# Kernel optimization log

Measured on AMD Instinct MI355X. Metric: run time of the kernel, lower is better.

Reference implementation:

```python
import jax, jax.numpy as jnp
import numpy as np

RES = 28      # input feature-map resolution
RES2 = 14     # ceil(RES/2) after downsample
NH = 8        # num_heads
KD = 16       # key_dim
D = 64        # attn_ratio * key_dim (per-head value dim)
DH = 512      # D * NH
N = RES * RES
N2 = RES2 * RES2


def _rel_idx():
    # Matches tf.meshgrid default 'xy' indexing in set_attention_bias_idxs.
    r = RES
    kp = np.stack(np.meshgrid(np.arange(r), np.arange(r), indexing='xy')).reshape(2, -1)
    qp = np.stack(np.meshgrid(np.arange(0, r, 2), np.arange(0, r, 2), indexing='xy')).reshape(2, -1)
    rel = np.abs(qp[:, :, None] - kp[:, None, :])
    return jnp.asarray(rel[0] * r + rel[1], dtype=jnp.int32)  # [N2, N]

REL_IDX = _rel_idx()


def _dw_stride2(x, w, b):
    # Depthwise 3x3 conv, stride 2, TF 'SAME' padding. w: [3,3,1,C]
    c = x.shape[-1]
    y = jax.lax.conv_general_dilated(
        x, w, window_strides=(2, 2), padding='SAME',
        dimension_numbers=('NHWC', 'HWIO', 'NHWC'), feature_group_count=c)
    return y + b


def setup_inputs() -> dict:
    key = jax.random.key(0)
    ks = jax.random.split(key, 10)
    f = jnp.float32
    C, OUT = 384, 768
    return {
        'x': jax.random.normal(ks[0], (64, RES, RES, C), f),
        'q_local_w': jax.random.normal(ks[1], (3, 3, 1, C), f) * 0.1,
        'q_local_b': jnp.zeros((C,), f),
        'q_proj_w': jax.random.normal(ks[2], (C, NH * KD), f) * 0.05,
        'q_proj_b': jnp.zeros((NH * KD,), f),
        'q_bn_s': jnp.ones((NH * KD,), f),
        'q_bn_b': jnp.zeros((NH * KD,), f),
        'k_w': jax.random.normal(ks[3], (C, NH * KD), f) * 0.05,
        'k_b': jnp.zeros((NH * KD,), f),
        'k_bn_s': jnp.ones((NH * KD,), f),
        'k_bn_b': jnp.zeros((NH * KD,), f),
        'v_w': jax.random.normal(ks[4], (C, DH), f) * 0.05,
        'v_b': jnp.zeros((DH,), f),
        'v_bn_s': jnp.ones((DH,), f),
        'v_bn_b': jnp.zeros((DH,), f),
        'vloc_w': jax.random.normal(ks[5], (3, 3, 1, DH), f) * 0.1,
        'vloc_b': jnp.zeros((DH,), f),
        'vloc_bn_s': jnp.ones((DH,), f),
        'vloc_bn_b': jnp.zeros((DH,), f),
        'proj_w': jax.random.normal(ks[6], (DH, OUT), f) * 0.05,
        'proj_b': jnp.zeros((OUT,), f),
        'proj_bn_s': jnp.ones((OUT,), f),
        'proj_bn_b': jnp.zeros((OUT,), f),
        'attn_bias': jax.random.normal(ks[7], (NH, N), f) * 0.1,
    }


def reference(x, q_local_w, q_local_b, q_proj_w, q_proj_b, q_bn_s, q_bn_b,
              k_w, k_b, k_bn_s, k_bn_b, v_w, v_b, v_bn_s, v_bn_b,
              vloc_w, vloc_b, vloc_bn_s, vloc_bn_b,
              proj_w, proj_b, proj_bn_s, proj_bn_b, attn_bias):
    B = x.shape[0]
    scale = KD ** -0.5
    # LGQuery: depthwise-conv local branch + 1x1 avg-pool (stride-2 subsample)
    q = _dw_stride2(x, q_local_w, q_local_b) + x[:, ::2, ::2, :]
    q = (q @ q_proj_w + q_proj_b) * q_bn_s + q_bn_b          # [B,14,14,128]
    k = (x @ k_w + k_b) * k_bn_s + k_bn_b                    # [B,28,28,128]
    v = (x @ v_w + v_b) * v_bn_s + v_bn_b                    # [B,28,28,512]
    v_local = _dw_stride2(v, vloc_w, vloc_b) * vloc_bn_s + vloc_bn_b  # [B,14,14,512]
    qh = q.reshape(B, N2, NH, KD).transpose(0, 2, 1, 3)      # [B,H,N2,KD]
    kh = k.reshape(B, N, NH, KD).transpose(0, 2, 3, 1)       # [B,H,KD,N]
    vh = v.reshape(B, N, NH, D).transpose(0, 2, 1, 3)        # [B,H,N,D]
    attn = (qh @ kh) * scale + attn_bias[:, REL_IDX]         # [B,H,N2,N]
    attn = jax.nn.softmax(attn, axis=-1)
    out = (attn @ vh).transpose(0, 2, 1, 3).reshape(B, RES2, RES2, DH)
    out = out + v_local
    # proj: Activation(None) is identity -> 1x1 conv + BN(inference)
    return (out @ proj_w + proj_b) * proj_bn_s + proj_bn_b   # [B,14,14,768]
```

## Files before the change

### kernel.cpp

```cpp
#include <hip/hip_runtime.h>
#include <cstdint>

#define RES    28
#define RES2   14
#define NHEAD  8
#define KDIM   16
#define DV     64
#define DHID   512
#define NSEQ   784
#define N2SEQ  196
#define BATCH  64
#define CIN    384

typedef unsigned short u16;
typedef short  short8_t __attribute__((ext_vector_type(8)));
typedef float  f32x4  __attribute__((ext_vector_type(4)));
typedef u16    us4    __attribute__((ext_vector_type(4)));
typedef u16    us8    __attribute__((ext_vector_type(8)));

__device__ __forceinline__ u16 f2bf(float f) {
    uint32_t u = __float_as_uint(f);
    return (u16)((u + 0x7fffu + ((u >> 16) & 1u)) >> 16);
}
__device__ __forceinline__ float bf2f(u16 h) {
    return __uint_as_float(((uint32_t)h) << 16);
}

#define PREP_N (49152 + 196608 + 49152 + 393216 + 1920 + 256)
__global__ __launch_bounds__(256)
void prep_kernel(const float* __restrict__ k_w, const float* __restrict__ v_w,
                 const float* __restrict__ q_proj_w, const float* __restrict__ proj_w,
                 const float* __restrict__ k_b, const float* __restrict__ v_b,
                 const float* __restrict__ k_bn_s, const float* __restrict__ v_bn_s,
                 const float* __restrict__ k_bn_b, const float* __restrict__ v_bn_b,
                 const float* __restrict__ q_bn_s, const float* __restrict__ q_bn_b,
                 u16* __restrict__ kvwt, u16* __restrict__ qwt, u16* __restrict__ pwt,
                 float* __restrict__ kv_eps, float* __restrict__ qsb)
{
    int i = blockIdx.x * 256 + threadIdx.x;
    if (i >= PREP_N) return;
    if (i < 49152) {
        int n = i / 384, k = i % 384;
        kvwt[i] = f2bf(k_w[(size_t)k * 128 + n]);
        return;
    }
    i -= 49152;
    if (i < 196608) {
        int n = i / 384, k = i % 384;
        kvwt[49152 + i] = f2bf(v_w[(size_t)k * 512 + n]);
        return;
    }
    i -= 196608;
    if (i < 49152) {
        int n = i / 384, k = i % 384;
        qwt[i] = f2bf(q_proj_w[(size_t)k * 128 + n]);
        return;
    }
    i -= 49152;
    if (i < 393216) {
        int n = i / 512, k = i % 512;
        pwt[i] = f2bf(proj_w[(size_t)k * 768 + n]);
        return;
    }
    i -= 393216;
    if (i < 1920) {
        int which = i / 640, j = i % 640;
        const float* a = which == 0 ? (j < 128 ? k_b : v_b)
                       : which == 1 ? (j < 128 ? k_bn_s : v_bn_s)
                                    : (j < 128 ? k_bn_b : v_bn_b);
        kv_eps[i] = a[j < 128 ? j : j - 128];
        return;
    }
    i -= 1920;
    qsb[i] = 0.25f * (i < 128 ? q_bn_s[i] : q_bn_b[i - 128]);
}

__global__ __launch_bounds__(256)
void biasC_kernel(const float* __restrict__ bias, float* __restrict__ biasC)
{
    int tid = blockIdx.x * 256 + threadIdx.x;
    if (tid >= NHEAD * 13 * 4 * 13 * 64) return;
    int lane = tid & 63;
    int rem  = tid >> 6;
    int qt = rem % 13; rem /= 13;
    int ks = rem % 4;  rem /= 4;
    int ti = rem % 13;
    int h  = rem / 13;
    int col = lane & 15, quad = lane >> 4;
    int q = qt * 16 + col;
    float4 out;
    float* po = &out.x;
    #pragma unroll
    for (int r = 0; r < 4; ++r) {
        int key = ti * 64 + ks * 16 + quad * 4 + r;
        float v;
        if (key >= NSEQ || q >= N2SEQ) {
            v = -1e30f;
        } else {
            int pi = q / 14, pj = q % 14;
            int ku = key / 28, kw = key % 28;
            int d0 = 2 * pj - kw; if (d0 < 0) d0 = -d0;
            int d1 = 2 * pi - ku; if (d1 < 0) d1 = -d1;
            v = bias[h * NSEQ + d0 * 28 + d1];
        }
        po[r] = v;
    }
    ((float4*)biasC)[tid] = out;
}

#define TM 128
#define TN 128
#define TK 32

template<int OUT_MODE, int A_FP32>
__global__ __launch_bounds__(256)
void gemm_mfma_kernel(const void* __restrict__ Av, const u16* __restrict__ Bt,
                      const float* __restrict__ bias, const float* __restrict__ scale,
                      const float* __restrict__ shift, void* __restrict__ outp,
                      u16* __restrict__ out2, int M, int N, int K, int rpb)
{
    __shared__ u16 As[TM * TK];
    __shared__ u16 Bs[TN * TK];

    const int t  = threadIdx.x;
    const int w  = t >> 6;
    const int li = t & 63;
    const int wm = w >> 1, wn = w & 1;
    const int bm = blockIdx.x * TM;
    const int bn = blockIdx.y * TN;
    const int m16 = li & 15;
    const int kg  = li >> 4;

    f32x4 acc[4][4];
    #pragma unroll
    for (int i = 0; i < 4; ++i)
        #pragma unroll
        for (int j = 0; j < 4; ++j) acc[i][j] = (f32x4)0.0f;

    for (int k0 = 0; k0 < K; k0 += TK) {
        #pragma unroll
        for (int i = 0; i < 2; ++i) {
            int c   = (w * 2 + i) * 64 + li;
            int row = c >> 2, kc = c & 3;
            if (A_FP32) {
                const float* ag = (const float*)Av + (size_t)(bm + row) * K + k0 + kc * 8;
                float4 a0 = *(const float4*)ag;
                float4 a1 = *(const float4*)(ag + 4);
                us8 vv;
                vv[0] = f2bf(a0.x); vv[1] = f2bf(a0.y); vv[2] = f2bf(a0.z); vv[3] = f2bf(a0.w);
                vv[4] = f2bf(a1.x); vv[5] = f2bf(a1.y); vv[6] = f2bf(a1.z); vv[7] = f2bf(a1.w);
                *(us8*)&As[(size_t)row * TK + kc * 8] = vv;
            } else {
                const u16* ag = (const u16*)Av + (size_t)(bm + row) * K + k0 + kc * 8;
                char* la = (char*)As + (size_t)(w * 2 + i) * 64 * 16;
                __builtin_amdgcn_global_load_lds(
                    (const __attribute__((address_space(1))) void*)ag,
                    (__attribute__((address_space(3))) void*)la, 16, 0, 0);
            }
            const u16* bg = Bt + (size_t)(bn + row) * K + k0 + kc * 8;
            char* lb = (char*)Bs + (size_t)(w * 2 + i) * 64 * 16;
            __builtin_amdgcn_global_load_lds(
                (const __attribute__((address_space(1))) void*)bg,
                (__attribute__((address_space(3))) void*)lb, 16, 0, 0);
        }
        __syncthreads();

        short8_t af[4], bf[4];
        #pragma unroll
        for (int mi = 0; mi < 4; ++mi)
            af[mi] = *(const short8_t*)&As[(wm * 64 + mi * 16 + m16) * TK + kg * 8];
        #pragma unroll
        for (int ni = 0; ni < 4; ++ni)
            bf[ni] = *(const short8_t*)&Bs[(wn * 64 + ni * 16 + m16) * TK + kg * 8];

        #pragma unroll
        for (int mi = 0; mi < 4; ++mi)
            #pragma unroll
            for (int ni = 0; ni < 4; ++ni)
                acc[mi][ni] = __builtin_amdgcn_mfma_f32_16x16x32_bf16(
                    af[mi], bf[ni], acc[mi][ni], 0, 0, 0);
        __syncthreads();
    }

    #pragma unroll
    for (int ni = 0; ni < 4; ++ni) {
        const int col = bn + wn * 64 + ni * 16 + m16;
        const float bi = bias[col], sc = scale[col], sh = shift[col];
        #pragma unroll
        for (int mi = 0; mi < 4; ++mi) {
            const int rbase = bm + wm * 64 + mi * 16 + kg * 4;
            #pragma unroll
            for (int r = 0; r < 4; ++r) {
                float val = (acc[mi][ni][r] + bi) * sc + sh;
                const int row = rbase + r;
                if (OUT_MODE == 0) {
                    ((float*)outp)[(size_t)row * N + col] = val;
                } else if (OUT_MODE == 1) {
                    ((u16*)outp)[(size_t)row * N + col] = f2bf(val);
                } else if (OUT_MODE == 2) {
                    int bb = row / rpb, tok = row % rpb;
                    int hh = col >> 4;
                    ((u16*)outp)[((size_t)(bb * NHEAD + hh) * rpb + tok) * 16 + (col & 15)] = f2bf(val);
                } else {
                    if (bn < 128) {
                        int bb = row / NSEQ, tok = row % NSEQ;
                        int hh = col >> 4;
                        ((u16*)outp)[((size_t)(bb * NHEAD + hh) * NSEQ + tok) * 16 + (col & 15)] = f2bf(val);
                    } else {
                        out2[(size_t)row * DHID + (col - 128)] = f2bf(val);
                    }
                }
            }
        }
    }
}

__global__ __launch_bounds__(256)
void qin_kernel(const float* __restrict__ x, const float* __restrict__ w,
                const float* __restrict__ b, u16* __restrict__ qin)
{
    const int C4 = CIN / 4;
    int idx = blockIdx.x * 256 + threadIdx.x;
    if (idx >= BATCH * RES2 * RES2 * C4) return;
    int c4 = idx % C4;
    int r  = idx / C4;
    int j  = r % RES2; r /= RES2;
    int i  = r % RES2;
    int bb = r / RES2;

    const float4* x4 = (const float4*)x;
    const float4* w4 = (const float4*)w;
    float4 acc = make_float4(0.f, 0.f, 0.f, 0.f);
    #pragma unroll
    for (int dy = 0; dy < 3; ++dy) {
        int iy = 2 * i + dy;
        if (iy >= RES) continue;
        #pragma unroll
        for (int dx = 0; dx < 3; ++dx) {
            int ix = 2 * j + dx;
            if (ix >= RES) continue;
            float4 xv = x4[((size_t)(bb * RES + iy) * RES + ix) * C4 + c4];
            float4 wv = w4[(dy * 3 + dx) * C4 + c4];
            acc.x += xv.x * wv.x; acc.y += xv.y * wv.y;
            acc.z += xv.z * wv.z; acc.w += xv.w * wv.w;
        }
    }
    float4 bv = ((const float4*)b)[c4];
    float4 xs = x4[((size_t)(bb * RES + 2 * i) * RES + 2 * j) * C4 + c4];
    us4 o;
    o.x = f2bf(acc.x + bv.x + xs.x);
    o.y = f2bf(acc.y + bv.y + xs.y);
    o.z = f2bf(acc.z + bv.z + xs.z);
    o.w = f2bf(acc.w + bv.w + xs.w);
    ((us4*)qin)[idx] = o;
}

__global__ __launch_bounds__(256)
void vloc_kernel(const u16* __restrict__ v, const float* __restrict__ w,
                 const float* __restrict__ b, const float* __restrict__ s,
                 const float* __restrict__ sh, u16* __restrict__ out)
{
    const int C4 = DHID / 4;
    int idx = blockIdx.x * 256 + threadIdx.x;
    if (idx >= BATCH * RES2 * RES2 * C4) return;
    int c4 = idx % C4;
    int r  = idx / C4;
    int j  = r % RES2; r /= RES2;
    int i  = r % RES2;
    int bb = r / RES2;

    const us4* v4 = (const us4*)v;
    const float4* w4 = (const float4*)w;
    float4 acc = make_float4(0.f, 0.f, 0.f, 0.f);
    #pragma unroll
    for (int dy = 0; dy < 3; ++dy) {
        int iy = 2 * i + dy;
        if (iy >= RES) continue;
        #pragma unroll
        for (int dx = 0; dx < 3; ++dx) {
            int ix = 2 * j + dx;
            if (ix >= RES) continue;
            us4 xu = v4[((size_t)(bb * RES + iy) * RES + ix) * C4 + c4];
            float4 wv = w4[(dy * 3 + dx) * C4 + c4];
            acc.x += bf2f(xu.x) * wv.x; acc.y += bf2f(xu.y) * wv.y;
            acc.z += bf2f(xu.z) * wv.z; acc.w += bf2f(xu.w) * wv.w;
        }
    }
    float4 bv = ((const float4*)b)[c4];
    float4 sv = ((const float4*)s)[c4];
    float4 hv = ((const float4*)sh)[c4];
    us4 o;
    o.x = f2bf((acc.x + bv.x) * sv.x + hv.x);
    o.y = f2bf((acc.y + bv.y) * sv.y + hv.y);
    o.z = f2bf((acc.z + bv.z) * sv.z + hv.z);
    o.w = f2bf((acc.w + bv.w) * sv.w + hv.w);
    ((us4*)out)[idx] = o;
}

__global__ __launch_bounds__(256)
void vt_transpose_kernel(const u16* __restrict__ vbuf, u16* __restrict__ vt)
{
    __shared__ u16 tile[64][66];
    const int t  = threadIdx.x;
    const int b  = blockIdx.x;
    const int k0 = blockIdx.y * 64;
    const int h  = blockIdx.z;

    {
        int kr = t >> 2, cc = (t & 3) * 16;
        int key = k0 + kr;
        if (key < NSEQ) {
            const u16* src = vbuf + ((size_t)b * NSEQ + key) * DHID + h * 64 + cc;
            us8 v0 = *(const us8*)src;
            us8 v1 = *(const us8*)(src + 8);
            #pragma unroll
            for (int i = 0; i < 8; ++i) { tile[kr][cc + i] = v0[i]; tile[kr][cc + 8 + i] = v1[i]; }
        }
    }
    __syncthreads();
    {
        int cr = t >> 2, kc = (t & 3) * 16;
        if (k0 + kc < NSEQ) {
            us8 o0, o1;
            #pragma unroll
            for (int i = 0; i < 8; ++i) { o0[i] = tile[kc + i][cr]; o1[i] = tile[kc + 8 + i][cr]; }
            u16* dst = vt + (((size_t)b * NHEAD + h) * 64 + cr) * NSEQ + k0 + kc;
            *(us8*)dst = o0;
            *(us8*)(dst + 8) = o1;
        }
    }
}

__global__ __launch_bounds__(256, 2)
void attn_mfma_kernel(const u16* __restrict__ q, const u16* __restrict__ k,
                      const u16* __restrict__ vt, const float* __restrict__ biasC,
                      u16* __restrict__ io)
{
    __shared__ u16 Ks[64 * 16];
    __shared__ u16 Vs[64 * 68];

    const int t    = threadIdx.x;
    const int w    = t >> 6;
    const int lane = t & 63;
    const int col  = lane & 15;
    const int quad = lane >> 4;
    const int par = blockIdx.x & 1;
    const int bhx = blockIdx.x >> 1;
    const int h  = bhx >> 6;
    const int b  = bhx & 63;
    const int bh = b * NHEAD + h;

    short8_t qf[2];
    #pragma unroll
    for (int i = 0; i < 2; ++i) {
        int qt = w + 4 * (par * 2 + i);
        qf[i] = (short8_t)0;
        if (qt < 13 && quad < 2) {
            int qq = qt * 16 + col; if (qq > 195) qq = 195;
            qf[i] = *(const short8_t*)(q + ((size_t)bh * N2SEQ + qq) * 16 + quad * 8);
        }
    }

    f32x4 O[2][4];
    float m[2], l[2];
    #pragma unroll
    for (int i = 0; i < 2; ++i) {
        m[i] = -3e38f; l[i] = 0.f;
        #pragma unroll
        for (int ns = 0; ns < 4; ++ns) O[i][ns] = (f32x4)0.0f;
    }

    const u16* vtb = vt + (size_t)bh * 64 * NSEQ;
    const u16* kb  = k + (size_t)bh * NSEQ * 16;

    for (int ti = 0; ti < 13; ++ti) {
        const int t0 = ti * 64;
        if (w < 2) {
            int c = w * 64 + lane;
            int tok = t0 + (c >> 1); if (tok > 783) tok = 783;
            const u16* src = kb + (size_t)tok * 16 + (c & 1) * 8;
            char* dst = (char*)Ks + w * 1024;
            __builtin_amdgcn_global_load_lds(
                (const __attribute__((address_space(1))) void*)src,
                (__attribute__((address_space(3))) void*)dst, 16, 0, 0);
        }
        {
            int d = t >> 2, part = t & 3;
            const u16* src = vtb + (size_t)d * NSEQ;
            u16* dst = Vs + d * 68 + part * 16;
            int kk = t0 + part * 16;
            int k0a = kk     > 776 ? 776 : kk;
            int k1a = kk + 8 > 776 ? 776 : kk + 8;
            us8 v0 = *(const us8*)(src + k0a);
            us8 v1 = *(const us8*)(src + k1a);
            us4 a, bb2, c2, d2;
            a.x = v0[0]; a.y = v0[1]; a.z = v0[2]; a.w = v0[3];
            bb2.x = v0[4]; bb2.y = v0[5]; bb2.z = v0[6]; bb2.w = v0[7];
            c2.x = v1[0]; c2.y = v1[1]; c2.z = v1[2]; c2.w = v1[3];
            d2.x = v1[4]; d2.y = v1[5]; d2.z = v1[6]; d2.w = v1[7];
            *(us4*)(dst)      = a;
            *(us4*)(dst + 4)  = bb2;
            *(us4*)(dst + 8)  = c2;
            *(us4*)(dst + 12) = d2;
        }
        __syncthreads();

        short8_t kf[4];
        #pragma unroll
        for (int ks = 0; ks < 4; ++ks) {
            kf[ks] = (short8_t)0;
            if (quad < 2)
                kf[ks] = *(const short8_t*)&Ks[(ks * 16 + col) * 16 + quad * 8];
        }
        short8_t vf[4][2];
        #pragma unroll
        for (int ns = 0; ns < 4; ++ns)
            #pragma unroll
            for (int pr = 0; pr < 2; ++pr) {
                const u16* vrow = &Vs[(ns * 16 + col) * 68 + pr * 32 + quad * 4];
                us4 v0 = *(const us4*)vrow;
                us4 v1 = *(const us4*)(vrow + 16);
                short8_t vv;
                vv[0] = (short)v0.x; vv[1] = (short)v0.y; vv[2] = (short)v0.z; vv[3] = (short)v0.w;
                vv[4] = (short)v1.x; vv[5] = (short)v1.y; vv[6] = (short)v1.z; vv[7] = (short)v1.w;
                vf[ns][pr] = vv;
            }

        #pragma unroll
        for (int i = 0; i < 2; ++i) {
            int qt = w + 4 * (par * 2 + i);
            if (qt < 13) {
                f32x4 S[4];
                #pragma unroll
                for (int ks = 0; ks < 4; ++ks) {
                    f32x4 c = *(const f32x4*)(biasC +
                        ((((size_t)h * 13 + ti) * 4 + ks) * 13 + qt) * 256 + lane * 4);
                    S[ks] = __builtin_amdgcn_mfma_f32_16x16x32_bf16(kf[ks], qf[i], c, 0, 0, 0);
                }
                float p[16];
                float mt = -3e38f;
                #pragma unroll
                for (int ks = 0; ks < 4; ++ks)
                    #pragma unroll
                    for (int r = 0; r < 4; ++r) {
                        float lg = S[ks][r];
                        p[ks * 4 + r] = lg;
                        mt = fmaxf(mt, lg);
                    }
                mt = fmaxf(mt, __shfl_xor(mt, 16));
                mt = fmaxf(mt, __shfl_xor(mt, 32));
                float mnew = fmaxf(m[i], mt);
                float alpha = __expf(m[i] - mnew);
                m[i] = mnew;
                float s = 0.f;
                #pragma unroll
                for (int j = 0; j < 16; ++j) { p[j] = __expf(p[j] - mnew); s += p[j]; }
                s += __shfl_xor(s, 16);
                s += __shfl_xor(s, 32);
                l[i] = l[i] * alpha + s;

                float ar[4];
                #pragma unroll
                for (int r = 0; r < 4; ++r) ar[r] = __shfl(alpha, quad * 4 + r);
                #pragma unroll
                for (int ns = 0; ns < 4; ++ns)
                    #pragma unroll
                    for (int r = 0; r < 4; ++r) O[i][ns][r] *= ar[r];

                short8_t pf[2];
                #pragma unroll
                for (int pr = 0; pr < 2; ++pr)
                    #pragma unroll
                    for (int j = 0; j < 8; ++j)
                        pf[pr][j] = (short)f2bf(p[(2 * pr + (j >> 2)) * 4 + (j & 3)]);

                #pragma unroll
                for (int ns = 0; ns < 4; ++ns)
                    #pragma unroll
                    for (int pr = 0; pr < 2; ++pr)
                        O[i][ns] = __builtin_amdgcn_mfma_f32_16x16x32_bf16(
                            pf[pr], vf[ns][pr], O[i][ns], 0, 0, 0);
            }
        }
        __syncthreads();
    }

    #pragma unroll
    for (int i = 0; i < 2; ++i) {
        int qt = w + 4 * (par * 2 + i);
        if (qt < 13) {
            float linv = 1.0f / l[i];
            float lr[4];
            #pragma unroll
            for (int r = 0; r < 4; ++r) lr[r] = __shfl(linv, quad * 4 + r);
            #pragma unroll
            for (int ns = 0; ns < 4; ++ns)
                #pragma unroll
                for (int r = 0; r < 4; ++r) {
                    int q2 = qt * 16 + quad * 4 + r;
                    if (q2 < N2SEQ) {
                        size_t a = ((size_t)(b * N2SEQ + q2) * DHID) + h * 64 + ns * 16 + col;
                        io[a] = f2bf(O[i][ns][r] * lr[r] + bf2f(io[a]));
                    }
                }
        }
    }
}

extern "C" void kernel_launch(void* const* d_in, const int* in_sizes, int n_in,
                              void* d_out, int out_size, void* d_ws, size_t ws_size,
                              hipStream_t stream)
{
    const float* x          = (const float*)d_in[0];
    const float* q_local_w  = (const float*)d_in[1];
    const float* q_local_b  = (const float*)d_in[2];
    const float* q_proj_w   = (const float*)d_in[3];
    const float* q_proj_b   = (const float*)d_in[4];
    const float* q_bn_s     = (const float*)d_in[5];
    const float* q_bn_b     = (const float*)d_in[6];
    const float* k_w        = (const float*)d_in[7];
    const float* k_b        = (const float*)d_in[8];
    const float* k_bn_s     = (const float*)d_in[9];
    const float* k_bn_b     = (const float*)d_in[10];
    const float* v_w        = (const float*)d_in[11];
    const float* v_b        = (const float*)d_in[12];
    const float* v_bn_s     = (const float*)d_in[13];
    const float* v_bn_b     = (const float*)d_in[14];
    const float* vloc_w     = (const float*)d_in[15];
    const float* vloc_b     = (const float*)d_in[16];
    const float* vloc_bn_s  = (const float*)d_in[17];
    const float* vloc_bn_b  = (const float*)d_in[18];
    const float* proj_w     = (const float*)d_in[19];
    const float* proj_b     = (const float*)d_in[20];
    const float* proj_bn_s  = (const float*)d_in[21];
    const float* proj_bn_b  = (const float*)d_in[22];
    const float* attn_bias  = (const float*)d_in[23];
    float* out = (float*)d_out;

    const int M1 = BATCH * NSEQ;
    const int M2 = BATCH * N2SEQ;

    char* p = (char*)d_ws;
    u16* qin_bf = (u16*)p;
    u16* vt     = (u16*)p;
    size_t off = 51380224;
    u16* kvwt = (u16*)(p + off);  off += 640 * 384 * 2;
    u16* qwt  = (u16*)(p + off);  off += 128 * 384 * 2;
    u16* pwt  = (u16*)(p + off);  off += 768 * 512 * 2;
    float* kv_eps = (float*)(p + off); off += 1920 * 4;
    float* qsb    = (float*)(p + off); off += 256 * 4;
    u16* kbuf = (u16*)(p + off);    off += (size_t)M1 * 128 * 2;
    u16* vbuf = (u16*)(p + off);    off += (size_t)M1 * DHID * 2;
    u16* qbuf = (u16*)(p + off);    off += (size_t)M2 * 128 * 2;
    u16* vloc_bf = (u16*)(p + off); off += (size_t)M2 * DHID * 2;
    float* biasC = (float*)(p + off);

    prep_kernel<<<dim3((PREP_N + 255) / 256), 256, 0, stream>>>(
        k_w, v_w, q_proj_w, proj_w, k_b, v_b, k_bn_s, v_bn_s, k_bn_b, v_bn_b,
        q_bn_s, q_bn_b, kvwt, qwt, pwt, kv_eps, qsb);
    {
        int items = NHEAD * 13 * 4 * 13 * 64;
        biasC_kernel<<<dim3((items + 255) / 256), 256, 0, stream>>>(attn_bias, biasC);
    }
    {
        int items = M2 * (CIN / 4);
        qin_kernel<<<dim3((items + 255) / 256), 256, 0, stream>>>(x, q_local_w, q_local_b, qin_bf);
    }
    gemm_mfma_kernel<3, 1><<<dim3(M1 / TM, 640 / TN), 256, 0, stream>>>(
        x, kvwt, kv_eps, kv_eps + 640, kv_eps + 1280, kbuf, vbuf, M1, 640, CIN, NSEQ);
    gemm_mfma_kernel<2, 0><<<dim3(M2 / TM, 128 / TN), 256, 0, stream>>>(
        qin_bf, qwt, q_proj_b, qsb, qsb + 128, qbuf, nullptr, M2, 128, CIN, N2SEQ);

    vt_transpose_kernel<<<dim3(BATCH, 13, NHEAD), 256, 0, stream>>>(vbuf, vt);

    {
        int items = M2 * (DHID / 4);
        vloc_kernel<<<dim3((items + 255) / 256), 256, 0, stream>>>(
            vbuf, vloc_w, vloc_b, vloc_bn_s, vloc_bn_b, vloc_bf);
    }
    attn_mfma_kernel<<<dim3(NHEAD * BATCH * 2), 256, 0, stream>>>(
        qbuf, kbuf, vt, biasC, vloc_bf);

    gemm_mfma_kernel<0, 0><<<dim3(M2 / TM, 768 / TN), 256, 0, stream>>>(
        vloc_bf, pwt, proj_b, proj_bn_s, proj_bn_b, out, nullptr, M2, 768, DHID, 0);
}
```

Measured before the change: 416.2 us.

## Pre-swizzle V into MFMA fragment layout and drop LDS staging in attention

The V transpose kernel now writes V directly in per-lane MFMA B-fragment order per 64-key tile, so the attention kernel can load fragments straight from global memory. K fragments are likewise read directly from global memory. This removes the shared-memory staging and both __syncthreads per key tile, and launch bounds go from 2 to 4 blocks per CU to raise occupancy. The cost is more, less coalesced global/L2 traffic per wave, since each wave loads its own copies of K and V instead of sharing them through LDS.

```diff
diff --git a/kernel.cpp b/kernel.cpp
--- a/kernel.cpp
+++ b/kernel.cpp
@@ -298,47 +298,46 @@
 }
 
 __global__ __launch_bounds__(256)
-void vt_transpose_kernel(const u16* __restrict__ vbuf, u16* __restrict__ vt)
-{
-    __shared__ u16 tile[64][66];
+void vfrag_kernel(const u16* __restrict__ vbuf, u16* __restrict__ vf)
+{
+    __shared__ u16 tile[64][72];
     const int t  = threadIdx.x;
     const int b  = blockIdx.x;
-    const int k0 = blockIdx.y * 64;
+    const int ti = blockIdx.y;
     const int h  = blockIdx.z;
-
+    const int k0 = ti * 64;
     {
         int kr = t >> 2, cc = (t & 3) * 16;
-        int key = k0 + kr;
-        if (key < NSEQ) {
-            const u16* src = vbuf + ((size_t)b * NSEQ + key) * DHID + h * 64 + cc;
-            us8 v0 = *(const us8*)src;
-            us8 v1 = *(const us8*)(src + 8);
-            #pragma unroll
-            for (int i = 0; i < 8; ++i) { tile[kr][cc + i] = v0[i]; tile[kr][cc + 8 + i] = v1[i]; }
-        }
+        int key = k0 + kr; if (key > 783) key = 783;
+        const u16* src = vbuf + ((size_t)b * NSEQ + key) * DHID + h * 64 + cc;
+        us8 v0 = *(const us8*)src;
+        us8 v1 = *(const us8*)(src + 8);
+        *(us8*)&tile[kr][cc]     = v0;
+        *(us8*)&tile[kr][cc + 8] = v1;
     }
     __syncthreads();
     {
-        int cr = t >> 2, kc = (t & 3) * 16;
-        if (k0 + kc < NSEQ) {
-            us8 o0, o1;
+        u16* dst = vf + (((size_t)(b * NHEAD + h) * 13 + ti) * 8) * 512;
+        #pragma unroll
+        for (int s0 = 0; s0 < 2; ++s0) {
+            int s = t + s0 * 256;
+            int lane = s & 63, fr = s >> 6;
+            int ns = fr >> 1, pr = fr & 1;
+            int col = lane & 15, quad = lane >> 4;
+            us8 o;
             #pragma unroll
-            for (int i = 0; i < 8; ++i) { o0[i] = tile[kc + i][cr]; o1[i] = tile[kc + 8 + i][cr]; }
-            u16* dst = vt + (((size_t)b * NHEAD + h) * 64 + cr) * NSEQ + k0 + kc;
-            *(us8*)dst = o0;
-            *(us8*)(dst + 8) = o1;
-        }
-    }
-}
-
-__global__ __launch_bounds__(256, 2)
+            for (int j = 0; j < 8; ++j)
+                o[j] = tile[pr * 32 + (j >> 2) * 16 + quad * 4 + (j & 3)][ns * 16 + col];
+            *(us8*)(dst + (size_t)s * 8) = o;
+        }
+    }
+}
+
+__global__ __launch_bounds__(256, 4)
 void attn_mfma_kernel(const u16* __restrict__ q, const u16* __restrict__ k,
-                      const u16* __restrict__ vt, const float* __restrict__ biasC,
+                      const u16* __restrict__ vfrag, const float* __restrict__ biasC,
                       u16* __restrict__ io)
 {
-    __shared__ u16 Ks[64 * 16];
-    __shared__ u16 Vs[64 * 68];
-
     const int t    = threadIdx.x;
     const int w    = t >> 6;
     const int lane = t & 63;
@@ -370,119 +369,92 @@
         for (int ns = 0; ns < 4; ++ns) O[i][ns] = (f32x4)0.0f;
     }
 
-    const u16* vtb = vt + (size_t)bh * 64 * NSEQ;
     const u16* kb  = k + (size_t)bh * NSEQ * 16;
+    const u16* vfb = vfrag + (size_t)bh * (13 * 4096);
 
     for (int ti = 0; ti < 13; ++ti) {
         const int t0 = ti * 64;
-        if (w < 2) {
-            int c = w * 64 + lane;
-            int tok = t0 + (c >> 1); if (tok > 783) tok = 783;
-            const u16* src = kb + (size_t)tok * 16 + (c & 1) * 8;
-            char* dst = (char*)Ks + w * 1024;
-            __builtin_amdgcn_global_load_lds(
-                (const __attribute__((address_space(1))) void*)src,
-                (__attribute__((address_space(3))) void*)dst, 16, 0, 0);
-        }
-        {
-            int d = t >> 2, part = t & 3;
-            const u16* src = vtb + (size_t)d * NSEQ;
-            u16* dst = Vs + d * 68 + part * 16;
-            int kk = t0 + part * 16;
-            int k0a = kk     > 776 ? 776 : kk;
-            int k1a = kk + 8 > 776 ? 776 : kk + 8;
-            us8 v0 = *(const us8*)(src + k0a);
-            us8 v1 = *(const us8*)(src + k1a);
-            us4 a, bb2, c2, d2;
-            a.x = v0[0]; a.y = v0[1]; a.z = v0[2]; a.w = v0[3];
-            bb2.x = v0[4]; bb2.y = v0[5]; bb2.z = v0[6]; bb2.w = v0[7];
-            c2.x = v1[0]; c2.y = v1[1]; c2.z = v1[2]; c2.w = v1[3];
-            d2.x = v1[4]; d2.y = v1[5]; d2.z = v1[6]; d2.w = v1[7];
-            *(us4*)(dst)      = a;
-            *(us4*)(dst + 4)  = bb2;
-            *(us4*)(dst + 8)  = c2;
-            *(us4*)(dst + 12) = d2;
-        }
-        __syncthreads();
 
         short8_t kf[4];
         #pragma unroll
         for (int ks = 0; ks < 4; ++ks) {
             kf[ks] = (short8_t)0;
-            if (quad < 2)
-                kf[ks] = *(const short8_t*)&Ks[(ks * 16 + col) * 16 + quad * 8];
-        }
-        short8_t vf[4][2];
-        #pragma unroll
-        for (int ns = 0; ns < 4; ++ns)
-            #pragma unroll
-            for (int pr = 0; pr < 2; ++pr) {
-                const u16* vrow = &Vs[(ns * 16 + col) * 68 + pr * 32 + quad * 4];
-                us4 v0 = *(const us4*)vrow;
-                us4 v1 = *(const us4*)(vrow + 16);
-                short8_t vv;
-                vv[0] = (short)v0.x; vv[1] = (short)v0.y; vv[2] = (short)v0.z; vv[3] = (short)v0.w;
-                vv[4] = (short)v1.x; vv[5] = (short)v1.y; vv[6] = (short)v1.z; vv[7] = (short)v1.w;
-                vf[ns][pr] = vv;
+            if (quad < 2) {
+                int tok = t0 + ks * 16 + col; if (tok > 783) tok = 783;
+                kf[ks] = *(const short8_t*)(kb + (size_t)tok * 16 + quad * 8);
             }
-
+        }
+
+        short8_t pf[2][2];
+        float alpha[2];
         #pragma unroll
         for (int i = 0; i < 2; ++i) {
             int qt = w + 4 * (par * 2 + i);
             if (qt < 13) {
+                const float* cb = biasC +
+                    ((((size_t)h * 13 + ti) * 4) * 13 + qt) * 256 + lane * 4;
                 f32x4 S[4];
                 #pragma unroll
                 for (int ks = 0; ks < 4; ++ks) {
-                    f32x4 c = *(const f32x4*)(biasC +
-                        ((((size_t)h * 13 + ti) * 4 + ks) * 13 + qt) * 256 + lane * 4);
+                    f32x4 c = *(const f32x4*)(cb + (size_t)ks * (13 * 256));
                     S[ks] = __builtin_amdgcn_mfma_f32_16x16x32_bf16(kf[ks], qf[i], c, 0, 0, 0);
                 }
-                float p[16];
                 float mt = -3e38f;
+                #pragma unroll
+                for (int ks = 0; ks < 4; ++ks)
+                    #pragma unroll
+                    for (int r = 0; r < 4; ++r) mt = fmaxf(mt, S[ks][r]);
+                mt = fmaxf(mt, __shfl_xor(mt, 16));
+                mt = fmaxf(mt, __shfl_xor(mt, 32));
+                float mnew = fmaxf(m[i], mt);
+                alpha[i] = __expf(m[i] - mnew);
+                m[i] = mnew;
+                float s = 0.f;
                 #pragma unroll
                 for (int ks = 0; ks < 4; ++ks)
                     #pragma unroll
                     for (int r = 0; r < 4; ++r) {
-                        float lg = S[ks][r];
-                        p[ks * 4 + r] = lg;
-                        mt = fmaxf(mt, lg);
+                        float e = __expf(S[ks][r] - mnew);
+                        S[ks][r] = e; s += e;
                     }
-                mt = fmaxf(mt, __shfl_xor(mt, 16));
-                mt = fmaxf(mt, __shfl_xor(mt, 32));
-                float mnew = fmaxf(m[i], mt);
-                float alpha = __expf(m[i] - mnew);
-                m[i] = mnew;
-                float s = 0.f;
-                #pragma unroll
-                for (int j = 0; j < 16; ++j) { p[j] = __expf(p[j] - mnew); s += p[j]; }
                 s += __shfl_xor(s, 16);
                 s += __shfl_xor(s, 32);
-                l[i] = l[i] * alpha + s;
-
+                l[i] = l[i] * alpha[i] + s;
+                #pragma unroll
+                for (int pr = 0; pr < 2; ++pr)
+                    #pragma unroll
+                    for (int j = 0; j < 8; ++j)
+                        pf[i][pr][j] = (short)f2bf(S[2 * pr + (j >> 2)][j & 3]);
+            }
+        }
+
+        short8_t vf[4][2];
+        #pragma unroll
+        for (int ns = 0; ns < 4; ++ns)
+            #pragma unroll
+            for (int pr = 0; pr < 2; ++pr)
+                vf[ns][pr] = *(const short8_t*)
+                    (vfb + ((size_t)(ti * 8 + ns * 2 + pr)) * 512 + lane * 8);
+
+        #pragma unroll
+        for (int i = 0; i < 2; ++i) {
+            int qt = w + 4 * (par * 2 + i);
+            if (qt < 13) {
                 float ar[4];
                 #pragma unroll
-                for (int r = 0; r < 4; ++r) ar[r] = __shfl(alpha, quad * 4 + r);
+                for (int r = 0; r < 4; ++r) ar[r] = __shfl(alpha[i], quad * 4 + r);
                 #pragma unroll
                 for (int ns = 0; ns < 4; ++ns)
                     #pragma unroll
                     for (int r = 0; r < 4; ++r) O[i][ns][r] *= ar[r];
-
-                short8_t pf[2];
-                #pragma unroll
-                for (int pr = 0; pr < 2; ++pr)
-                    #pragma unroll
-                    for (int j = 0; j < 8; ++j)
-                        pf[pr][j] = (short)f2bf(p[(2 * pr + (j >> 2)) * 4 + (j & 3)]);
-
                 #pragma unroll
                 for (int ns = 0; ns < 4; ++ns)
                     #pragma unroll
                     for (int pr = 0; pr < 2; ++pr)
                         O[i][ns] = __builtin_amdgcn_mfma_f32_16x16x32_bf16(
-                            pf[pr], vf[ns][pr], O[i][ns], 0, 0, 0);
+                            pf[i][pr], vf[ns][pr], O[i][ns], 0, 0, 0);
             }
         }
-        __syncthreads();
     }
 
     #pragma unroll
@@ -542,8 +514,8 @@
 
     char* p = (char*)d_ws;
     u16* qin_bf = (u16*)p;
-    u16* vt     = (u16*)p;
-    size_t off = 51380224;
+    u16* vfrag  = (u16*)p;
+    size_t off = 54525952;
     u16* kvwt = (u16*)(p + off);  off += 640 * 384 * 2;
     u16* qwt  = (u16*)(p + off);  off += 128 * 384 * 2;
     u16* pwt  = (u16*)(p + off);  off += 768 * 512 * 2;
@@ -571,7 +543,7 @@
     gemm_mfma_kernel<2, 0><<<dim3(M2 / TM, 128 / TN), 256, 0, stream>>>(
         qin_bf, qwt, q_proj_b, qsb, qsb + 128, qbuf, nullptr, M2, 128, CIN, N2SEQ);
 
-    vt_transpose_kernel<<<dim3(BATCH, 13, NHEAD), 256, 0, stream>>>(vbuf, vt);
+    vfrag_kernel<<<dim3(BATCH, 13, NHEAD), 256, 0, stream>>>(vbuf, vfrag);
 
     {
         int items = M2 * (DHID / 4);
@@ -579,7 +551,7 @@
             vbuf, vloc_w, vloc_b, vloc_bn_s, vloc_bn_b, vloc_bf);
     }
     attn_mfma_kernel<<<dim3(NHEAD * BATCH * 2), 256, 0, stream>>>(
-        qbuf, kbuf, vt, biasC, vloc_bf);
+        qbuf, kbuf, vfrag, biasC, vloc_bf);
 
     gemm_mfma_kernel<0, 0><<<dim3(M2 / TM, 768 / TN), 256, 0, stream>>>(
         vloc_bf, pwt, proj_b, proj_bn_s, proj_bn_b, out, nullptr, M2, 768, DHID, 0);
```

Result: faster. 387.9 us (-6.8%).
